# Kernel optimization log

Hardware: AMD Instinct MI355X
Metric: run time of the kernel (lower is better)

The kernel has to match this reference:

```python
import jax, jax.numpy as jnp
import numpy as np

NE, NR, D, B = 1_000_000, 1000, 32, 1_048_576
CURV = 1.0  # curvature K
HALF = D // 2


def _project(spatial):
    # recompute time component so point lies on hyperboloid <x,x>_L = -1/K
    x0 = jnp.sqrt(1.0 / CURV + jnp.sum(spatial * spatial, axis=-1, keepdims=True))
    return jnp.concatenate([x0, spatial], axis=-1)


def _lorentz_inner(u, v):
    return -u[..., 0] * v[..., 0] + jnp.sum(u[..., 1:] * v[..., 1:], axis=-1)


def setup_inputs() -> dict:
    key = jax.random.key(0)
    k0, k1, k2, k3, k4, k5, k6, k7 = jax.random.split(key, 8)
    tangent = jax.random.normal(k0, (NE, D), dtype=jnp.float32) * 0.01
    x0 = jnp.sqrt(1.0 / CURV + jnp.sum(tangent * tangent, axis=-1, keepdims=True))
    entity_emb = jnp.concatenate([x0, tangent], axis=-1)  # [NE, D+1]
    rel_boost_w = jax.random.normal(k1, (NR, D), dtype=jnp.float32) * 0.01
    rel_rot_w = jax.random.normal(k2, (NR, D), dtype=jnp.float32) * 0.01  # torch init is zeros; small noise for a nontrivial test
    rel_trans_w = jax.random.normal(k3, (NR, D), dtype=jnp.float32) * 0.01
    ent_bias_w = jax.random.normal(k4, (NE, 1), dtype=jnp.float32) * 0.01
    heads = jax.random.randint(k5, (B,), 0, NE)
    relations = jax.random.randint(k6, (B,), 0, NR)
    tails = jax.random.randint(k7, (B,), 0, NE)
    return {"heads": heads, "relations": relations, "tails": tails,
            "entity_emb": entity_emb, "rel_boost_w": rel_boost_w,
            "rel_rot_w": rel_rot_w, "rel_trans_w": rel_trans_w,
            "ent_bias_w": ent_bias_w}


def reference(heads, relations, tails, entity_emb, rel_boost_w, rel_rot_w, rel_trans_w, ent_bias_w):
    h = entity_emb[heads]                      # [B, D+1]
    t = entity_emb[tails]                      # [B, D+1]
    boost = rel_boost_w[relations]             # [B, D]
    rotation = rel_rot_w[relations]            # [B, D]
    translation = rel_trans_w[relations]       # [B, D]

    # --- spatial rotation: pairwise Givens rotations (i, i+HALF) ---
    x0 = h[..., 0:1]
    sp = h[..., 1:]
    a, b = sp[..., :HALF], sp[..., HALF:]
    c = jnp.cos(rotation[..., :HALF])
    s = jnp.sin(rotation[..., :HALF])
    rotated = jnp.concatenate([c * a - s * b, s * a + c * b], axis=-1)
    h_rot = jnp.concatenate([x0, rotated], axis=-1)

    # --- Lorentz boost along first spatial axis (only rapidity[..., 0] used) ---
    rap = jnp.clip(boost, -2.0, 2.0)
    c0 = jnp.cosh(rap[..., 0:1])
    s0 = jnp.sinh(rap[..., 0:1])
    bx0 = h_rot[..., 0:1]
    bx1 = h_rot[..., 1:2]
    new_x1 = bx0 * s0 + bx1 * c0
    new_spatial = jnp.concatenate([new_x1, h_rot[..., 2:]], axis=-1)
    h_boost = _project(new_spatial)  # time component recomputed by projection

    # --- exp map with tangent v = 0.1 * [0, translation] ---
    v = jnp.concatenate([jnp.zeros_like(translation[..., 0:1]), translation], axis=-1) * 0.1
    vn = jnp.sqrt(jnp.clip(_lorentz_inner(v, v), 1e-6, None))[..., None]
    res = jnp.cosh(vn) * h_boost + jnp.sinh(vn) * v / vn
    h_trans = _project(res[..., 1:])

    # --- Lorentz distance and score ---
    inner = _lorentz_inner(h_trans, t)
    ic = jnp.clip(-inner * CURV, 1.0 + 1e-6, None)
    dist = (1.0 / np.sqrt(CURV)) * jnp.arccosh(ic)
    b_h = ent_bias_w[heads][..., 0]
    b_t = ent_bias_w[tails][..., 0]
    return -dist * dist + b_h + b_t
```

## Files before the change

### kernel.cpp

```cpp
#include <hip/hip_runtime.h>
#include <hip/hip_fp16.h>
#include <math.h>

#define NR_ 1000
#define NE_ 1000000
#define D_ 32
#define HALF_ 16
#define EMB_DIM 33
#define TAB_STRIDE 68
#define LROW 17
#define WSLOT (64 * LROW)
#define H16_BYTES ((size_t)NE_ * 64)
#define REPACK_BLOCKS 62500

__global__ __launch_bounds__(256) void prep_kernel(
    const float* __restrict__ emb, const float* __restrict__ boost_w,
    const float* __restrict__ rot_w, const float* __restrict__ trans_w,
    unsigned int* __restrict__ h16, float* __restrict__ tab) {
  const int b = blockIdx.x;
  if (b < REPACK_BLOCKS) {
    int t = b * 256 + threadIdx.x;
    int r = t >> 4, j = t & 15;
    const float* p = emb + (size_t)r * EMB_DIM + 1 + 2 * j;
    union { __half2 h; unsigned int u; } cvt;
    cvt.h = __half2(__float2half_rn(p[0]), __float2half_rn(p[1]));
    h16[t] = cvt.u;
    return;
  }
  int r = (b - REPACK_BLOCKS) * 256 + threadIdx.x;
  if (r >= NR_) return;
  const float* ro = rot_w   + (size_t)r * D_;
  const float* tr = trans_w + (size_t)r * D_;
  float* o = tab + (size_t)r * TAB_STRIDE;
  #pragma unroll
  for (int j = 0; j < HALF_; ++j) {
    float th = ro[j];
    o[j]         = cosf(th);
    o[HALF_ + j] = sinf(th);
  }
  float s2 = 0.f;
  #pragma unroll
  for (int j = 0; j < D_; ++j) { float v = tr[j]; s2 = fmaf(v, v, s2); }
  float vn  = sqrtf(fmaxf(0.01f * s2, 1e-6f));
  float k   = sinhf(vn) / vn * 0.1f;
  #pragma unroll
  for (int j = 0; j < D_; ++j) o[2 * HALF_ + j] = k * tr[j];
  float rap = fminf(fmaxf(boost_w[(size_t)r * D_], -2.f), 2.f);
  o[64] = coshf(rap);
  o[65] = sinhf(rap);
  o[66] = coshf(vn);
  o[67] = 0.f;
}

__global__ __launch_bounds__(256) void lorentz_mlp_kernel(
    const int* __restrict__ heads, const int* __restrict__ rels,
    const int* __restrict__ tails, const unsigned int* __restrict__ h16,
    const float* __restrict__ bias, const float* __restrict__ tab,
    float* __restrict__ out, int n) {
  __shared__ unsigned int buf[4][2 * WSLOT];

  const int lane = threadIdx.x & 63;
  const int w    = threadIdx.x >> 6;
  const int gid  = blockIdx.x * 256 + threadIdx.x;
  const int i    = (gid < n) ? gid : (n - 1);

  const int hd = heads[i];
  const int rl = rels[i];
  const int tl = tails[i];
  const float bsum = bias[hd] + bias[tl];
  const float4* __restrict__ T =
      reinterpret_cast<const float4*>(tab + (size_t)rl * TAB_STRIDE);

  unsigned int* __restrict__ hb = buf[w];
  unsigned int* __restrict__ tb = buf[w] + WSLOT;
  const int esub = lane >> 2;
  const int q    = lane & 3;

  #pragma unroll
  for (int k = 0; k < 4; ++k) {
    const int e   = k * 16 + esub;
    const int row = __shfl(hd, e, 64);
    const uint4 v = *reinterpret_cast<const uint4*>(
        h16 + (size_t)row * 16 + q * 4);
    unsigned int* dst = hb + e * LROW + q * 4;
    dst[0] = v.x; dst[1] = v.y; dst[2] = v.z; dst[3] = v.w;
  }
  #pragma unroll
  for (int k = 0; k < 4; ++k) {
    const int e   = k * 16 + esub;
    const int row = __shfl(tl, e, 64);
    const uint4 v = *reinterpret_cast<const uint4*>(
        h16 + (size_t)row * 16 + q * 4);
    unsigned int* dst = tb + e * LROW + q * 4;
    dst[0] = v.x; dst[1] = v.y; dst[2] = v.z; dst[3] = v.w;
  }

  const unsigned int* __restrict__ myh = hb + lane * LROW;
  union U2 { unsigned int u; __half2 h; };
  float a[HALF_], b[HALF_];
  #pragma unroll
  for (int uu = 0; uu < 8; ++uu) {
    U2 ua; ua.u = myh[uu];
    U2 ub; ub.u = myh[8 + uu];
    float2 fa = __half22float2(ua.h);
    float2 fb = __half22float2(ub.h);
    a[2 * uu] = fa.x; a[2 * uu + 1] = fa.y;
    b[2 * uu] = fb.x; b[2 * uu + 1] = fb.y;
  }
  float r[D_];
  float hsq = 0.f;
  #pragma unroll
  for (int qq = 0; qq < 4; ++qq) {
    float4 cv = T[qq];
    float4 sv = T[4 + qq];
    float cj[4] = {cv.x, cv.y, cv.z, cv.w};
    float sj[4] = {sv.x, sv.y, sv.z, sv.w};
    #pragma unroll
    for (int m = 0; m < 4; ++m) {
      int j = 4 * qq + m;
      hsq = fmaf(a[j], a[j], fmaf(b[j], b[j], hsq));
      r[j]         = cj[m] * a[j] - sj[m] * b[j];
      r[HALF_ + j] = sj[m] * a[j] + cj[m] * b[j];
    }
  }
  const float x0 = sqrtf(1.f + hsq);
  float4 hv4 = T[16];
  r[0] = fmaf(x0, hv4.y, r[0] * hv4.x);
  const float cvn = hv4.z;

  float rs[D_];
  float n2 = 0.f;
  #pragma unroll
  for (int qq = 0; qq < 8; ++qq) {
    float4 kv = T[8 + qq];
    float kj[4] = {kv.x, kv.y, kv.z, kv.w};
    #pragma unroll
    for (int m = 0; m < 4; ++m) {
      int j = 4 * qq + m;
      rs[j] = fmaf(cvn, r[j], kj[m]);
      n2 = fmaf(rs[j], rs[j], n2);
    }
  }
  const float ht0 = sqrtf(1.f + n2);

  const unsigned int* __restrict__ myt = tb + lane * LROW;
  float dot = 0.f, tsq = 0.f;
  #pragma unroll
  for (int uu = 0; uu < 16; ++uu) {
    U2 ut; ut.u = myt[uu];
    float2 ft = __half22float2(ut.h);
    dot = fmaf(rs[2 * uu], ft.x, fmaf(rs[2 * uu + 1], ft.y, dot));
    tsq = fmaf(ft.x, ft.x, fmaf(ft.y, ft.y, tsq));
  }
  const float t0 = sqrtf(1.f + tsq);

  float neg_inner = fmaf(ht0, t0, -dot);
  float ic   = fmaxf(neg_inner, 1.0f + 1e-6f);
  float dist = acoshf(ic);
  if (gid < n) out[gid] = bsum - dist * dist;
}

__global__ __launch_bounds__(256) void lorentz_fallback_kernel(
    const int* __restrict__ heads, const int* __restrict__ rels,
    const int* __restrict__ tails, const float* __restrict__ emb,
    const float* __restrict__ boost_w, const float* __restrict__ rot_w,
    const float* __restrict__ trans_w, const float* __restrict__ bias,
    float* __restrict__ out, int n) {
  int i = blockIdx.x * blockDim.x + threadIdx.x;
  if (i >= n) return;
  int hd = heads[i], rl = rels[i], tl = tails[i];
  const float* hrow = emb + (size_t)hd * EMB_DIM;
  const float* trow = emb + (size_t)tl * EMB_DIM;
  const float* ro = rot_w   + (size_t)rl * D_;
  const float* tr = trans_w + (size_t)rl * D_;
  float c[HALF_], s[HALF_], kt[D_];
  #pragma unroll
  for (int j = 0; j < HALF_; ++j) { float th = ro[j]; c[j] = cosf(th); s[j] = sinf(th); }
  float s2 = 0.f;
  #pragma unroll
  for (int j = 0; j < D_; ++j) { float v = tr[j]; s2 = fmaf(v, v, s2); }
  float vn = sqrtf(fmaxf(0.01f * s2, 1e-6f));
  float cvn = coshf(vn);
  float k = sinhf(vn) / vn * 0.1f;
  #pragma unroll
  for (int j = 0; j < D_; ++j) kt[j] = k * tr[j];
  float rap = fminf(fmaxf(boost_w[(size_t)rl * D_], -2.f), 2.f);
  float c0 = coshf(rap), s0 = sinhf(rap);
  float x0 = hrow[0];
  float r[D_];
  #pragma unroll
  for (int j = 0; j < HALF_; ++j) {
    float a = hrow[1 + j], b = hrow[1 + HALF_ + j];
    r[j] = c[j] * a - s[j] * b;
    r[HALF_ + j] = s[j] * a + c[j] * b;
  }
  r[0] = fmaf(x0, s0, r[0] * c0);
  float t0 = trow[0], n2 = 0.f, dot = 0.f;
  #pragma unroll
  for (int j = 0; j < D_; ++j) {
    float rsv = fmaf(cvn, r[j], kt[j]);
    n2  = fmaf(rsv, rsv, n2);
    dot = fmaf(rsv, trow[1 + j], dot);
  }
  float ht0 = sqrtf(1.f + n2);
  float neg_inner = fmaf(ht0, t0, -dot);
  float ic = fmaxf(neg_inner, 1.0f + 1e-6f);
  float dist = acoshf(ic);
  out[i] = bias[hd] + bias[tl] - dist * dist;
}

extern "C" void kernel_launch(void* const* d_in, const int* in_sizes, int n_in,
                              void* d_out, int out_size, void* d_ws, size_t ws_size,
                              hipStream_t stream) {
  const int*   heads  = (const int*)d_in[0];
  const int*   rels   = (const int*)d_in[1];
  const int*   tails  = (const int*)d_in[2];
  const float* emb    = (const float*)d_in[3];
  const float* boostw = (const float*)d_in[4];
  const float* rotw   = (const float*)d_in[5];
  const float* transw = (const float*)d_in[6];
  const float* bias   = (const float*)d_in[7];
  float* out = (float*)d_out;
  int n = in_sizes[0];

  const size_t tab_bytes = (size_t)NR_ * TAB_STRIDE * sizeof(float);
  dim3 block(256);
  dim3 grid((n + 255) / 256);

  if (ws_size >= H16_BYTES + tab_bytes) {
    unsigned int* h16 = (unsigned int*)d_ws;
    float* tab = (float*)((char*)d_ws + H16_BYTES);
    prep_kernel<<<dim3(REPACK_BLOCKS + 4), block, 0, stream>>>(
        emb, boostw, rotw, transw, h16, tab);
    lorentz_mlp_kernel<<<grid, block, 0, stream>>>(
        heads, rels, tails, h16, bias, tab, out, n);
  } else {
    lorentz_fallback_kernel<<<grid, block, 0, stream>>>(
        heads, rels, tails, emb, boostw, rotw, transw, bias, out, n);
  }
}
```

Baseline: 292.5 us.

## Split each triple across four lanes with shuffle reductions; vectorize fp16 repack

The main kernel now assigns four lanes to each triple. Each lane loads one 16-byte slice of the head and tail fp16 rows directly and computes a quarter of the rotation, exp-map and dot products, then combines the partial sums with xor shuffles. This removes the shared-memory staging pass and cuts per-thread register pressure, at the cost of four times as many threads, redundant index and bias loads per lane, and extra shuffles. The prep repack also changes from one half2 per thread to four per thread, using nontemporal loads and a single 16-byte store.

```diff
diff --git a/kernel.cpp b/kernel.cpp
--- a/kernel.cpp
+++ b/kernel.cpp
@@ -8,10 +8,8 @@
 #define HALF_ 16
 #define EMB_DIM 33
 #define TAB_STRIDE 68
-#define LROW 17
-#define WSLOT (64 * LROW)
 #define H16_BYTES ((size_t)NE_ * 64)
-#define REPACK_BLOCKS 62500
+#define REPACK_BLOCKS 15625
 
 __global__ __launch_bounds__(256) void prep_kernel(
     const float* __restrict__ emb, const float* __restrict__ boost_w,
@@ -20,11 +18,24 @@
   const int b = blockIdx.x;
   if (b < REPACK_BLOCKS) {
     int t = b * 256 + threadIdx.x;
-    int r = t >> 4, j = t & 15;
-    const float* p = emb + (size_t)r * EMB_DIM + 1 + 2 * j;
-    union { __half2 h; unsigned int u; } cvt;
-    cvt.h = __half2(__float2half_rn(p[0]), __float2half_rn(p[1]));
-    h16[t] = cvt.u;
+    int r = t >> 2, q = t & 3;
+    const float* pa = emb + (size_t)r * EMB_DIM + 1 + 4 * q;
+    const float* pb = pa + HALF_;
+    float a0 = __builtin_nontemporal_load(pa + 0);
+    float a1 = __builtin_nontemporal_load(pa + 1);
+    float a2 = __builtin_nontemporal_load(pa + 2);
+    float a3 = __builtin_nontemporal_load(pa + 3);
+    float b0 = __builtin_nontemporal_load(pb + 0);
+    float b1 = __builtin_nontemporal_load(pb + 1);
+    float b2 = __builtin_nontemporal_load(pb + 2);
+    float b3 = __builtin_nontemporal_load(pb + 3);
+    union { __half2 h; unsigned int u; } c0, c1, c2, c3;
+    c0.h = __half2(__float2half_rn(a0), __float2half_rn(a1));
+    c1.h = __half2(__float2half_rn(a2), __float2half_rn(a3));
+    c2.h = __half2(__float2half_rn(b0), __float2half_rn(b1));
+    c3.h = __half2(__float2half_rn(b2), __float2half_rn(b3));
+    uint4 v = make_uint4(c0.u, c1.u, c2.u, c3.u);
+    *reinterpret_cast<uint4*>(h16 + (size_t)r * 16 + 4 * q) = v;
     return;
   }
   int r = (b - REPACK_BLOCKS) * 256 + threadIdx.x;
@@ -52,112 +63,107 @@
   o[67] = 0.f;
 }
 
-__global__ __launch_bounds__(256) void lorentz_mlp_kernel(
+__global__ __launch_bounds__(256) void lorentz_coop_kernel(
     const int* __restrict__ heads, const int* __restrict__ rels,
     const int* __restrict__ tails, const unsigned int* __restrict__ h16,
     const float* __restrict__ bias, const float* __restrict__ tab,
     float* __restrict__ out, int n) {
-  __shared__ unsigned int buf[4][2 * WSLOT];
-
-  const int lane = threadIdx.x & 63;
-  const int w    = threadIdx.x >> 6;
-  const int gid  = blockIdx.x * 256 + threadIdx.x;
-  const int i    = (gid < n) ? gid : (n - 1);
+  const int q = threadIdx.x & 3;
+  const int e = (blockIdx.x * 256 + threadIdx.x) >> 2;
+  const int i = (e < n) ? e : (n - 1);
 
   const int hd = heads[i];
   const int rl = rels[i];
   const int tl = tails[i];
-  const float bsum = bias[hd] + bias[tl];
+
+  const uint4 hv = *reinterpret_cast<const uint4*>(h16 + (size_t)hd * 16 + 4 * q);
+  const uint4 tv = *reinterpret_cast<const uint4*>(h16 + (size_t)tl * 16 + 4 * q);
+
   const float4* __restrict__ T =
       reinterpret_cast<const float4*>(tab + (size_t)rl * TAB_STRIDE);
-
-  unsigned int* __restrict__ hb = buf[w];
-  unsigned int* __restrict__ tb = buf[w] + WSLOT;
-  const int esub = lane >> 2;
-  const int q    = lane & 3;
-
-  #pragma unroll
-  for (int k = 0; k < 4; ++k) {
-    const int e   = k * 16 + esub;
-    const int row = __shfl(hd, e, 64);
-    const uint4 v = *reinterpret_cast<const uint4*>(
-        h16 + (size_t)row * 16 + q * 4);
-    unsigned int* dst = hb + e * LROW + q * 4;
-    dst[0] = v.x; dst[1] = v.y; dst[2] = v.z; dst[3] = v.w;
-  }
-  #pragma unroll
-  for (int k = 0; k < 4; ++k) {
-    const int e   = k * 16 + esub;
-    const int row = __shfl(tl, e, 64);
-    const uint4 v = *reinterpret_cast<const uint4*>(
-        h16 + (size_t)row * 16 + q * 4);
-    unsigned int* dst = tb + e * LROW + q * 4;
-    dst[0] = v.x; dst[1] = v.y; dst[2] = v.z; dst[3] = v.w;
-  }
-
-  const unsigned int* __restrict__ myh = hb + lane * LROW;
+  const float4 cq = T[q];
+  const float4 sq = T[4 + q];
+  const float4 ka = T[8 + q];
+  const float4 kb = T[12 + q];
+  const float4 hp = T[16];
+  const float bsum = bias[hd] + bias[tl];
+
   union U2 { unsigned int u; __half2 h; };
-  float a[HALF_], b[HALF_];
-  #pragma unroll
-  for (int uu = 0; uu < 8; ++uu) {
-    U2 ua; ua.u = myh[uu];
-    U2 ub; ub.u = myh[8 + uu];
-    float2 fa = __half22float2(ua.h);
-    float2 fb = __half22float2(ub.h);
-    a[2 * uu] = fa.x; a[2 * uu + 1] = fa.y;
-    b[2 * uu] = fb.x; b[2 * uu + 1] = fb.y;
-  }
-  float r[D_];
-  float hsq = 0.f;
-  #pragma unroll
-  for (int qq = 0; qq < 4; ++qq) {
-    float4 cv = T[qq];
-    float4 sv = T[4 + qq];
-    float cj[4] = {cv.x, cv.y, cv.z, cv.w};
-    float sj[4] = {sv.x, sv.y, sv.z, sv.w};
-    #pragma unroll
-    for (int m = 0; m < 4; ++m) {
-      int j = 4 * qq + m;
-      hsq = fmaf(a[j], a[j], fmaf(b[j], b[j], hsq));
-      r[j]         = cj[m] * a[j] - sj[m] * b[j];
-      r[HALF_ + j] = sj[m] * a[j] + cj[m] * b[j];
-    }
-  }
+  U2 u0, u1, u2, u3;
+  u0.u = hv.x; u1.u = hv.y; u2.u = hv.z; u3.u = hv.w;
+  const float2 fa01 = __half22float2(u0.h);
+  const float2 fa23 = __half22float2(u1.h);
+  const float2 fb01 = __half22float2(u2.h);
+  const float2 fb23 = __half22float2(u3.h);
+  const float a0 = fa01.x, a1 = fa01.y, a2 = fa23.x, a3 = fa23.y;
+  const float b0 = fb01.x, b1 = fb01.y, b2 = fb23.x, b3 = fb23.y;
+
+  float hsq = a0 * a0;
+  hsq = fmaf(a1, a1, hsq); hsq = fmaf(a2, a2, hsq); hsq = fmaf(a3, a3, hsq);
+  hsq = fmaf(b0, b0, hsq); hsq = fmaf(b1, b1, hsq);
+  hsq = fmaf(b2, b2, hsq); hsq = fmaf(b3, b3, hsq);
+  hsq += __shfl_xor(hsq, 1);
+  hsq += __shfl_xor(hsq, 2);
   const float x0 = sqrtf(1.f + hsq);
-  float4 hv4 = T[16];
-  r[0] = fmaf(x0, hv4.y, r[0] * hv4.x);
-  const float cvn = hv4.z;
-
-  float rs[D_];
-  float n2 = 0.f;
-  #pragma unroll
-  for (int qq = 0; qq < 8; ++qq) {
-    float4 kv = T[8 + qq];
-    float kj[4] = {kv.x, kv.y, kv.z, kv.w};
-    #pragma unroll
-    for (int m = 0; m < 4; ++m) {
-      int j = 4 * qq + m;
-      rs[j] = fmaf(cvn, r[j], kj[m]);
-      n2 = fmaf(rs[j], rs[j], n2);
-    }
-  }
+
+  float rA0 = cq.x * a0 - sq.x * b0;
+  float rA1 = cq.y * a1 - sq.y * b1;
+  float rA2 = cq.z * a2 - sq.z * b2;
+  float rA3 = cq.w * a3 - sq.w * b3;
+  const float rB0 = fmaf(sq.x, a0, cq.x * b0);
+  const float rB1 = fmaf(sq.y, a1, cq.y * b1);
+  const float rB2 = fmaf(sq.z, a2, cq.z * b2);
+  const float rB3 = fmaf(sq.w, a3, cq.w * b3);
+
+  if (q == 0) rA0 = fmaf(x0, hp.y, rA0 * hp.x);
+  const float cvn = hp.z;
+
+  const float sA0 = fmaf(cvn, rA0, ka.x);
+  const float sA1 = fmaf(cvn, rA1, ka.y);
+  const float sA2 = fmaf(cvn, rA2, ka.z);
+  const float sA3 = fmaf(cvn, rA3, ka.w);
+  const float sB0 = fmaf(cvn, rB0, kb.x);
+  const float sB1 = fmaf(cvn, rB1, kb.y);
+  const float sB2 = fmaf(cvn, rB2, kb.z);
+  const float sB3 = fmaf(cvn, rB3, kb.w);
+
+  float n2 = sA0 * sA0;
+  n2 = fmaf(sA1, sA1, n2); n2 = fmaf(sA2, sA2, n2); n2 = fmaf(sA3, sA3, n2);
+  n2 = fmaf(sB0, sB0, n2); n2 = fmaf(sB1, sB1, n2);
+  n2 = fmaf(sB2, sB2, n2); n2 = fmaf(sB3, sB3, n2);
+  n2 += __shfl_xor(n2, 1);
+  n2 += __shfl_xor(n2, 2);
   const float ht0 = sqrtf(1.f + n2);
 
-  const unsigned int* __restrict__ myt = tb + lane * LROW;
-  float dot = 0.f, tsq = 0.f;
-  #pragma unroll
-  for (int uu = 0; uu < 16; ++uu) {
-    U2 ut; ut.u = myt[uu];
-    float2 ft = __half22float2(ut.h);
-    dot = fmaf(rs[2 * uu], ft.x, fmaf(rs[2 * uu + 1], ft.y, dot));
-    tsq = fmaf(ft.x, ft.x, fmaf(ft.y, ft.y, tsq));
-  }
+  U2 w0, w1, w2, w3;
+  w0.u = tv.x; w1.u = tv.y; w2.u = tv.z; w3.u = tv.w;
+  const float2 ta01 = __half22float2(w0.h);
+  const float2 ta23 = __half22float2(w1.h);
+  const float2 tb01 = __half22float2(w2.h);
+  const float2 tb23 = __half22float2(w3.h);
+
+  float dot = sA0 * ta01.x;
+  dot = fmaf(sA1, ta01.y, dot); dot = fmaf(sA2, ta23.x, dot);
+  dot = fmaf(sA3, ta23.y, dot);
+  dot = fmaf(sB0, tb01.x, dot); dot = fmaf(sB1, tb01.y, dot);
+  dot = fmaf(sB2, tb23.x, dot); dot = fmaf(sB3, tb23.y, dot);
+
+  float tsq = ta01.x * ta01.x;
+  tsq = fmaf(ta01.y, ta01.y, tsq); tsq = fmaf(ta23.x, ta23.x, tsq);
+  tsq = fmaf(ta23.y, ta23.y, tsq);
+  tsq = fmaf(tb01.x, tb01.x, tsq); tsq = fmaf(tb01.y, tb01.y, tsq);
+  tsq = fmaf(tb23.x, tb23.x, tsq); tsq = fmaf(tb23.y, tb23.y, tsq);
+
+  dot += __shfl_xor(dot, 1);
+  dot += __shfl_xor(dot, 2);
+  tsq += __shfl_xor(tsq, 1);
+  tsq += __shfl_xor(tsq, 2);
   const float t0 = sqrtf(1.f + tsq);
 
-  float neg_inner = fmaf(ht0, t0, -dot);
-  float ic   = fmaxf(neg_inner, 1.0f + 1e-6f);
-  float dist = acoshf(ic);
-  if (gid < n) out[gid] = bsum - dist * dist;
+  const float neg_inner = fmaf(ht0, t0, -dot);
+  const float ic = fmaxf(neg_inner, 1.0f + 1e-6f);
+  const float dist = acoshf(ic);
+  if (q == 0 && e < n) out[e] = bsum - dist * dist;
 }
 
 __global__ __launch_bounds__(256) void lorentz_fallback_kernel(
@@ -225,16 +231,17 @@
 
   const size_t tab_bytes = (size_t)NR_ * TAB_STRIDE * sizeof(float);
   dim3 block(256);
-  dim3 grid((n + 255) / 256);
 
   if (ws_size >= H16_BYTES + tab_bytes) {
     unsigned int* h16 = (unsigned int*)d_ws;
     float* tab = (float*)((char*)d_ws + H16_BYTES);
     prep_kernel<<<dim3(REPACK_BLOCKS + 4), block, 0, stream>>>(
         emb, boostw, rotw, transw, h16, tab);
-    lorentz_mlp_kernel<<<grid, block, 0, stream>>>(
+    dim3 grid_main((n + 63) / 64);
+    lorentz_coop_kernel<<<grid_main, block, 0, stream>>>(
         heads, rels, tails, h16, bias, tab, out, n);
   } else {
+    dim3 grid((n + 255) / 256);
     lorentz_fallback_kernel<<<grid, block, 0, stream>>>(
         heads, rels, tails, emb, boostw, rotw, transw, bias, out, n);
   }
```

Result: faster. 280.6 us (-4.1%).
